# Kernel tuning notes

Measured on AMD Instinct MI355X. Metric: run time of the kernel, lower is better.

Reference implementation:

```python
import jax, jax.numpy as jnp
import numpy as np

# per-amino-acid residue lengths (heavy atoms - 1), 20 types, sorted ascending for readability
RES_LEN_NP = np.array([3, 4, 5, 5, 6, 6, 6, 7, 7, 7, 7, 7, 8, 8, 8, 9, 10, 10, 11, 13], dtype=np.int32)
LMAX = int(RES_LEN_NP.max())  # 13
N_TYPES = 20
N_RES = 2048
BATCH = 16
DV_ATM = 64
DV_AMN = 64


def _atoms_for(seq_types_np):
    return int(RES_LEN_NP[seq_types_np].sum())


def setup_inputs() -> dict:
    key = jax.random.key(0)
    k1, k2, k3, k4 = jax.random.split(key, 4)
    seq_np = (np.arange(N_RES) % N_TYPES).astype(np.int32)
    atoms = _atoms_for(seq_np)  # 15036
    pos_atm = jax.random.normal(k1, (BATCH, atoms, 3), dtype=jnp.float32)
    pos_amn = jax.random.normal(k2, (BATCH, N_RES, 3), dtype=jnp.float32)
    scale = 1.0 / np.sqrt(LMAX)
    W_amn = jax.random.normal(k3, (N_TYPES, DV_AMN, LMAX), dtype=jnp.float32) * scale
    W_atm = jax.random.normal(k4, (N_TYPES, LMAX, DV_ATM, LMAX), dtype=jnp.float32) * scale
    return {
        "pos_atm": pos_atm,
        "pos_amn": pos_amn,
        "W_amn": W_amn,
        "W_atm": W_atm,
        "seq_types": jnp.asarray(seq_np),
    }


def reference(pos_atm, pos_amn, W_amn, W_atm, seq_types):
    """Vectorized equivalent of the per-residue loop:
    for each residue i of type t with length L_t:
      diff = pos_atm[:, start_i:start_i+L_t] - pos_amn[:, i, None]        # (B, L_t, 3)
      x_v_amn[:, i] = einsum('ol,bld->bod', W_amn[t, :, :L_t], diff)       # (B, Damn, 3)
      x_v_atm block  = einsum('mvl,bld->bmvd', W_atm[t, :L_t, :, :L_t], diff)
    Residues are padded to LMAX and batched; padding is masked out.
    """
    res_len = jnp.asarray(RES_LEN_NP)
    B, atoms, _ = pos_atm.shape
    lens = res_len[seq_types]                                  # (N,)
    starts = jnp.concatenate([jnp.zeros((1,), lens.dtype), jnp.cumsum(lens)[:-1]])
    ar = jnp.arange(LMAX, dtype=lens.dtype)
    atom_idx = jnp.clip(starts[:, None] + ar[None, :], 0, atoms - 1)  # (N, LMAX)
    mask = ar[None, :] < lens[:, None]                                 # (N, LMAX)

    # diffs: (B, N, LMAX, 3), zeroed at padding
    diffs = (pos_atm[:, atom_idx] - pos_amn[:, :, None, :]) * mask[None, :, :, None]

    Wa = W_amn[seq_types]                                      # (N, Damn, LMAX)
    x_v_amn = jnp.einsum('bnld,nol->bnod', diffs, Wa)          # (B, N, Damn, 3)

    Wt = W_atm[seq_types]                                      # (N, LMAX, Dv, LMAX)
    xa = jnp.einsum('bnld,nmvl->bnmvd', diffs, Wt)             # (B, N, LMAX, Dv, 3)
    xa = xa * mask[None, :, :, None, None]

    # scatter padded per-residue atom outputs back to the flat atom axis;
    # invalid slots go to a dummy row `atoms` that is sliced off
    idx = jnp.where(mask, atom_idx, atoms).reshape(-1)         # (N*LMAX,)
    xa_flat = xa.reshape(B, -1, DV_ATM, 3)                     # (B, N*LMAX, Dv, 3)
    x_v_atm = jnp.zeros((B, atoms + 1, DV_ATM, 3), pos_atm.dtype).at[:, idx].add(xa_flat)[:, :atoms]
    return x_v_atm, x_v_amn
```

## Files before the change

### kernel.cpp

```cpp
#include <hip/hip_runtime.h>

#define N_RES 2048
#define BATCH 16
#define LMAX  13
#define NSLOT 14
#define DV    64
#define VSTR  68

__device__ __constant__ int RES_LEN_D[20] = {3,4,5,5,6,6,6,7,7,7,7,7,8,8,8,9,10,10,11,13};

__global__ __launch_bounds__(256, 3)
void posmix_kernel(const float* __restrict__ pos_atm,
                   const float* __restrict__ pos_amn,
                   const float* __restrict__ W_amn,
                   const float* __restrict__ W_atm,
                   const int*   __restrict__ seq,
                   float* __restrict__ out_atm,
                   float* __restrict__ out_amn,
                   int atoms)
{
  const int i   = blockIdx.x;
  const int tid = threadIdx.x;
  const int t   = seq[i];
  const int L   = RES_LEN_D[t];

  __shared__ __align__(16) float w_lds[NSLOT * LMAX * VSTR];
  __shared__ __align__(16) float diff_lds[BATCH * 40];

  int* red = (int*)diff_lds;
  {
    int s = 0;
    int base = tid * 8;
    #pragma unroll
    for (int k = 0; k < 8; ++k) {
      int r = base + k;
      if (r < i) s += RES_LEN_D[seq[r]];
    }
    red[tid] = s;
  }
  __syncthreads();
  #pragma unroll
  for (int off = 128; off > 0; off >>= 1) {
    if (tid < off) red[tid] += red[tid + off];
    __syncthreads();
  }
  const int start = red[0];
  __syncthreads();

  {
    const float* Wt = W_atm + (size_t)t * (LMAX * DV * LMAX);
    const float* Wa = W_amn + (size_t)t * (DV * LMAX);
    const int total = (L + 1) * (DV * LMAX);
    for (int g = tid; g < total; g += 256) {
      int m = g / (DV * LMAX);
      int r = g - m * (DV * LMAX);
      int v = r / LMAX;
      int l = r - v * LMAX;
      const float* src = (m < L) ? (Wt + (size_t)m * (DV * LMAX)) : Wa;
      w_lds[(m * LMAX + l) * VSTR + v] = src[r];
    }
  }

  if (tid < BATCH * LMAX) {
    int b = tid / LMAX;
    int l = tid - b * LMAX;
    float dx = 0.f, dy = 0.f, dz = 0.f;
    if (l < L) {
      const float* pa = pos_atm + ((size_t)b * atoms + (size_t)(start + l)) * 3;
      const float* pm = pos_amn + ((size_t)b * N_RES + i) * 3;
      dx = pa[0] - pm[0];
      dy = pa[1] - pm[1];
      dz = pa[2] - pm[2];
    }
    float* dd = diff_lds + b * 40 + l * 3;
    dd[0] = dx; dd[1] = dy; dd[2] = dz;
  }
  if (tid < BATCH) diff_lds[tid * 40 + 39] = 0.f;
  __syncthreads();

  const int b  = tid >> 4;
  const int va = tid & 15;

  float df[40] __attribute__((aligned(16)));
  {
    const float4* s4 = (const float4*)(diff_lds + b * 40);
    float4* d4 = (float4*)df;
    #pragma unroll
    for (int k = 0; k < 10; ++k) d4[k] = s4[k];
  }

  const float* wbase = w_lds + 4 * va;

  for (int m = 0; m <= L; ++m) {
    const float* wr = wbase + (m * LMAX) * VSTR;

    float acc[12];
    #pragma unroll
    for (int j = 0; j < 12; ++j) acc[j] = 0.f;

    #pragma unroll
    for (int l = 0; l < LMAX; ++l) {
      float4 w = *(const float4*)(wr + l * VSTR);
      float dx = df[3*l + 0], dy = df[3*l + 1], dz = df[3*l + 2];
      acc[0]  += w.x * dx; acc[1]  += w.x * dy; acc[2]  += w.x * dz;
      acc[3]  += w.y * dx; acc[4]  += w.y * dy; acc[5]  += w.y * dz;
      acc[6]  += w.z * dx; acc[7]  += w.z * dy; acc[8]  += w.z * dz;
      acc[9]  += w.w * dx; acc[10] += w.w * dy; acc[11] += w.w * dz;
    }

    float* dst = (m < L)
      ? out_atm + ((size_t)b * atoms + (size_t)(start + m)) * 192 + va * 12
      : out_amn + ((size_t)b * N_RES + i) * 192 + va * 12;
    *(float4*)(dst + 0) = make_float4(acc[0], acc[1],  acc[2],  acc[3]);
    *(float4*)(dst + 4) = make_float4(acc[4], acc[5],  acc[6],  acc[7]);
    *(float4*)(dst + 8) = make_float4(acc[8], acc[9],  acc[10], acc[11]);
  }
}

extern "C" void kernel_launch(void* const* d_in, const int* in_sizes, int n_in,
                              void* d_out, int out_size, void* d_ws, size_t ws_size,
                              hipStream_t stream) {
  const float* pos_atm = (const float*)d_in[0];
  const float* pos_amn = (const float*)d_in[1];
  const float* W_amn   = (const float*)d_in[2];
  const float* W_atm   = (const float*)d_in[3];
  const int*   seq     = (const int*)d_in[4];

  const int atoms = in_sizes[0] / (BATCH * 3);
  float* out_atm = (float*)d_out;
  float* out_amn = out_atm + (size_t)BATCH * atoms * DV * 3;

  posmix_kernel<<<N_RES, 256, 0, stream>>>(pos_atm, pos_amn, W_amn, W_atm, seq,
                                           out_atm, out_amn, atoms);
}
```

Baseline: 245.3 us.

## Pretranspose weights and precompute residue starts in a prep kernel

Adds a prep kernel that transposes per-type weights into a v-contiguous global layout and computes residue start offsets with a block prefix scan. The main kernel drops its per-block LDS weight staging, strided transpose and 2048-wide reduction, and instead reads float4 weights directly from global memory/L2. The diff values also move into registers without a local array. This removes redundant per-block setup work at the cost of an extra launch and repeated global weight reads that rely on cache hits.

```diff
diff --git a/kernel.cpp b/kernel.cpp
--- a/kernel.cpp
+++ b/kernel.cpp
@@ -5,16 +5,61 @@
 #define LMAX  13
 #define NSLOT 14
 #define DV    64
-#define VSTR  68
+#define WT_FLOATS (20 * NSLOT * LMAX * DV)
+#define WT_BYTES  (WT_FLOATS * 4)
 
 __device__ __constant__ int RES_LEN_D[20] = {3,4,5,5,6,6,6,7,7,7,7,7,8,8,8,9,10,10,11,13};
 
-__global__ __launch_bounds__(256, 3)
+__global__ __launch_bounds__(256)
+void prep_kernel(const float* __restrict__ W_amn,
+                 const float* __restrict__ W_atm,
+                 const int*   __restrict__ seq,
+                 float* __restrict__ WT,
+                 int*   __restrict__ starts)
+{
+  const int blk = blockIdx.x;
+  const int tid = threadIdx.x;
+
+  if (blk < 20 * NSLOT) {
+    const int t = blk / NSLOT;
+    const int s = blk - t * NSLOT;
+    const float* src = (s < LMAX)
+        ? W_atm + ((size_t)t * LMAX + s) * (DV * LMAX)
+        : W_amn + (size_t)t * (DV * LMAX);
+    float* dst = WT + (size_t)blk * (LMAX * DV);
+    for (int g = tid; g < LMAX * DV; g += 256) {
+      int l = g >> 6;
+      int v = g & 63;
+      dst[g] = src[v * LMAX + l];
+    }
+  } else {
+    __shared__ int ssum[256];
+    const int base = tid * 8;
+    int le[8];
+    int s = 0;
+    #pragma unroll
+    for (int k = 0; k < 8; ++k) { le[k] = RES_LEN_D[seq[base + k]]; s += le[k]; }
+    ssum[tid] = s;
+    __syncthreads();
+    #pragma unroll
+    for (int off = 1; off < 256; off <<= 1) {
+      int v = (tid >= off) ? ssum[tid - off] : 0;
+      __syncthreads();
+      ssum[tid] += v;
+      __syncthreads();
+    }
+    int run = ssum[tid] - s;
+    #pragma unroll
+    for (int k = 0; k < 8; ++k) { starts[base + k] = run; run += le[k]; }
+  }
+}
+
+__global__ __launch_bounds__(256, 4)
 void posmix_kernel(const float* __restrict__ pos_atm,
                    const float* __restrict__ pos_amn,
-                   const float* __restrict__ W_amn,
-                   const float* __restrict__ W_atm,
                    const int*   __restrict__ seq,
+                   const float* __restrict__ WT,
+                   const int*   __restrict__ starts,
                    float* __restrict__ out_atm,
                    float* __restrict__ out_amn,
                    int atoms)
@@ -23,43 +68,9 @@
   const int tid = threadIdx.x;
   const int t   = seq[i];
   const int L   = RES_LEN_D[t];
+  const int start = starts[i];
 
-  __shared__ __align__(16) float w_lds[NSLOT * LMAX * VSTR];
   __shared__ __align__(16) float diff_lds[BATCH * 40];
-
-  int* red = (int*)diff_lds;
-  {
-    int s = 0;
-    int base = tid * 8;
-    #pragma unroll
-    for (int k = 0; k < 8; ++k) {
-      int r = base + k;
-      if (r < i) s += RES_LEN_D[seq[r]];
-    }
-    red[tid] = s;
-  }
-  __syncthreads();
-  #pragma unroll
-  for (int off = 128; off > 0; off >>= 1) {
-    if (tid < off) red[tid] += red[tid + off];
-    __syncthreads();
-  }
-  const int start = red[0];
-  __syncthreads();
-
-  {
-    const float* Wt = W_atm + (size_t)t * (LMAX * DV * LMAX);
-    const float* Wa = W_amn + (size_t)t * (DV * LMAX);
-    const int total = (L + 1) * (DV * LMAX);
-    for (int g = tid; g < total; g += 256) {
-      int m = g / (DV * LMAX);
-      int r = g - m * (DV * LMAX);
-      int v = r / LMAX;
-      int l = r - v * LMAX;
-      const float* src = (m < L) ? (Wt + (size_t)m * (DV * LMAX)) : Wa;
-      w_lds[(m * LMAX + l) * VSTR + v] = src[r];
-    }
-  }
 
   if (tid < BATCH * LMAX) {
     int b = tid / LMAX;
@@ -81,39 +92,48 @@
   const int b  = tid >> 4;
   const int va = tid & 15;
 
-  float df[40] __attribute__((aligned(16)));
-  {
-    const float4* s4 = (const float4*)(diff_lds + b * 40);
-    float4* d4 = (float4*)df;
-    #pragma unroll
-    for (int k = 0; k < 10; ++k) d4[k] = s4[k];
-  }
+  const float4* s4 = (const float4*)(diff_lds + b * 40);
+  const float4 d0 = s4[0], d1 = s4[1], d2 = s4[2], d3 = s4[3], d4 = s4[4];
+  const float4 d5 = s4[5], d6 = s4[6], d7 = s4[7], d8 = s4[8], d9 = s4[9];
 
-  const float* wbase = w_lds + 4 * va;
+  const float4* wt4 = (const float4*)WT + (size_t)(t * NSLOT) * (LMAX * 16) + va;
+
+  float* outb_atm = out_atm + ((size_t)b * atoms + (size_t)start) * 192 + va * 12;
+  float* outb_amn = out_amn + ((size_t)b * N_RES + i) * 192 + va * 12;
 
   for (int m = 0; m <= L; ++m) {
-    const float* wr = wbase + (m * LMAX) * VSTR;
+    const int sl = (m < L) ? m : 13;
+    const float4* wr = wt4 + (size_t)sl * (LMAX * 16);
 
     float acc[12];
     #pragma unroll
     for (int j = 0; j < 12; ++j) acc[j] = 0.f;
 
-    #pragma unroll
-    for (int l = 0; l < LMAX; ++l) {
-      float4 w = *(const float4*)(wr + l * VSTR);
-      float dx = df[3*l + 0], dy = df[3*l + 1], dz = df[3*l + 2];
-      acc[0]  += w.x * dx; acc[1]  += w.x * dy; acc[2]  += w.x * dz;
-      acc[3]  += w.y * dx; acc[4]  += w.y * dy; acc[5]  += w.y * dz;
-      acc[6]  += w.z * dx; acc[7]  += w.z * dy; acc[8]  += w.z * dz;
-      acc[9]  += w.w * dx; acc[10] += w.w * dy; acc[11] += w.w * dz;
-    }
+    #define STEP(LI, DX_, DY_, DZ_) { float4 w = wr[(LI) * 16]; \
+      acc[0]  += w.x * DX_; acc[1]  += w.x * DY_; acc[2]  += w.x * DZ_; \
+      acc[3]  += w.y * DX_; acc[4]  += w.y * DY_; acc[5]  += w.y * DZ_; \
+      acc[6]  += w.z * DX_; acc[7]  += w.z * DY_; acc[8]  += w.z * DZ_; \
+      acc[9]  += w.w * DX_; acc[10] += w.w * DY_; acc[11] += w.w * DZ_; }
 
-    float* dst = (m < L)
-      ? out_atm + ((size_t)b * atoms + (size_t)(start + m)) * 192 + va * 12
-      : out_amn + ((size_t)b * N_RES + i) * 192 + va * 12;
-    *(float4*)(dst + 0) = make_float4(acc[0], acc[1],  acc[2],  acc[3]);
-    *(float4*)(dst + 4) = make_float4(acc[4], acc[5],  acc[6],  acc[7]);
-    *(float4*)(dst + 8) = make_float4(acc[8], acc[9],  acc[10], acc[11]);
+    STEP(0,  d0.x, d0.y, d0.z)
+    STEP(1,  d0.w, d1.x, d1.y)
+    STEP(2,  d1.z, d1.w, d2.x)
+    STEP(3,  d2.y, d2.z, d2.w)
+    STEP(4,  d3.x, d3.y, d3.z)
+    STEP(5,  d3.w, d4.x, d4.y)
+    STEP(6,  d4.z, d4.w, d5.x)
+    STEP(7,  d5.y, d5.z, d5.w)
+    STEP(8,  d6.x, d6.y, d6.z)
+    STEP(9,  d6.w, d7.x, d7.y)
+    STEP(10, d7.z, d7.w, d8.x)
+    STEP(11, d8.y, d8.z, d8.w)
+    STEP(12, d9.x, d9.y, d9.z)
+    #undef STEP
+
+    float* dst = (m < L) ? (outb_atm + (size_t)m * 192) : outb_amn;
+    ((float4*)dst)[0] = make_float4(acc[0], acc[1],  acc[2],  acc[3]);
+    ((float4*)dst)[1] = make_float4(acc[4], acc[5],  acc[6],  acc[7]);
+    ((float4*)dst)[2] = make_float4(acc[8], acc[9],  acc[10], acc[11]);
   }
 }
 
@@ -130,6 +150,10 @@
   float* out_atm = (float*)d_out;
   float* out_amn = out_atm + (size_t)BATCH * atoms * DV * 3;
 
-  posmix_kernel<<<N_RES, 256, 0, stream>>>(pos_atm, pos_amn, W_amn, W_atm, seq,
+  float* WT     = (float*)d_ws;
+  int*   starts = (int*)((char*)d_ws + WT_BYTES);
+
+  prep_kernel<<<20 * NSLOT + 1, 256, 0, stream>>>(W_amn, W_atm, seq, WT, starts);
+  posmix_kernel<<<N_RES, 256, 0, stream>>>(pos_atm, pos_amn, seq, WT, starts,
                                            out_atm, out_amn, atoms);
 }
```

After: 368.4 us. +50.2%, slower.
